# Performance work log

Hardware: AMD Instinct MI355X
Metric: run time of the kernel (lower is better)

## Reference

```python
import math
import jax, jax.numpy as jnp
from jax import lax
import numpy as np

N_LAYERS = 16
MAX_DIL = 128
C_RES = 64
C_DIL = 128
ENC_F = 256
ENC_S = 256
LOOP = int(math.floor(math.log2(MAX_DIL))) + 1  # 8
DILS = [2 ** (i % LOOP) for i in range(N_LAYERS)]  # 1..128 twice


def setup_inputs() -> dict:
    key = jax.random.key(0)
    ks = jax.random.split(key, 9)
    B, T = 8, 131072
    signal = jax.random.normal(ks[0], (B, 1, T), dtype=jnp.float32)
    # params (xavier-ish scales ~ 1/sqrt(fan_in+fan_out))
    W0 = jax.random.normal(ks[1], (C_RES, 1), dtype=jnp.float32) * 0.5          # 1x1 input conv
    b0 = jax.random.normal(ks[2], (C_RES,), dtype=jnp.float32) * 0.02
    Wd = jax.random.normal(ks[3], (N_LAYERS, C_DIL, C_RES, 2), dtype=jnp.float32) * 0.08  # k=2 dilated convs
    bd = jax.random.normal(ks[4], (N_LAYERS, C_DIL), dtype=jnp.float32) * 0.02
    Wr = jax.random.normal(ks[5], (N_LAYERS, C_RES, C_DIL), dtype=jnp.float32) * 0.08     # 1x1 residual convs
    br = jax.random.normal(ks[6], (N_LAYERS, C_RES), dtype=jnp.float32) * 0.02
    Wf = jax.random.normal(ks[7], (1, C_RES), dtype=jnp.float32) * 0.1          # 1x1 final conv
    bf = jax.random.normal(ks[8], (1,), dtype=jnp.float32) * 0.02
    return {"signal": signal, "W0": W0, "b0": b0, "Wd": Wd, "bd": bd,
            "Wr": Wr, "br": br, "Wf": Wf, "bf": bf}


def reference(signal, W0, b0, Wd, bd, Wr, br, Wf, bf):
    # input 1x1 conv: [B,1,T] -> [B,C_RES,T]
    x = jnp.einsum('oi,bit->bot', W0, signal) + b0[None, :, None]
    for i, d in enumerate(DILS):
        skip = x
        h = jax.nn.relu(x)
        # kernel-2 dilated conv, VALID (no causal pad in original): len shrinks by d
        L = h.shape[2]
        h = (jnp.einsum('oc,bct->bot', Wd[i, :, :, 0], h[:, :, :L - d])
             + jnp.einsum('oc,bct->bot', Wd[i, :, :, 1], h[:, :, d:])
             + bd[i][None, :, None])
        h = jax.nn.relu(h)
        # 1x1 residual conv back to C_RES
        h = jnp.einsum('oc,bct->bot', Wr[i], h) + br[i][None, :, None]
        # residual add with right-aligned trim of skip
        x = h + skip[:, :, skip.shape[2] - h.shape[2]:]
    # final 1x1 conv -> [B,1,L']
    x = jnp.einsum('oc,bct->bot', Wf, x) + bf[None, :, None]
    # AvgPool1d(ENC_F, stride=ENC_S), VALID, count_include_pad irrelevant (no pad)
    x = lax.reduce_window(x, 0.0, lax.add, (1, 1, ENC_F), (1, 1, ENC_S), 'VALID') / ENC_F
    return x
```

## Files before the change

### kernel.cpp

```cpp
#include <hip/hip_runtime.h>
#include <hip/hip_bf16.h>
#include <stdint.h>

typedef __attribute__((ext_vector_type(8))) short short8;
typedef __attribute__((ext_vector_type(4))) float f32x4;
typedef unsigned short bfu;

#define T_TILE  128
#define RING    384
#define NTILES  8
#define NLAYERS 16
#define T0LEN   131072
#define BATCH   8
#define RFIELD  510
#define FINLEN  130560
#define CHCAP   65280

#define BARRIER() asm volatile("s_waitcnt lgkmcnt(0)\n\ts_barrier" ::: "memory")

__device__ __forceinline__ bfu f2bf(float f) {
    unsigned u = __float_as_uint(f);
    u += 0x7FFFu + ((u >> 16) & 1u);
    return (bfu)(u >> 16);
}
__device__ __forceinline__ unsigned pk2(float a, float b) {
    __hip_bfloat16 lo = __float2bfloat16(a);
    __hip_bfloat16 hi = __float2bfloat16(b);
    unsigned short ul = __builtin_bit_cast(unsigned short, lo);
    unsigned short uh = __builtin_bit_cast(unsigned short, hi);
    return (unsigned)ul | ((unsigned)uh << 16);
}
__device__ __forceinline__ float bf2f(bfu h) { return __uint_as_float(((unsigned)h) << 16); }
__device__ __forceinline__ unsigned relu2(unsigned w) {
    return w & ~(((w >> 15) & 0x00010001u) * 0xFFFFu);
}

__global__ void prep_weights(const float* __restrict__ Wd, const float* __restrict__ Wr,
                             bfu* __restrict__ wcat, bfu* __restrict__ wrb)
{
    int idx = blockIdx.x * 256 + threadIdx.x;
    const int total1 = NLAYERS * 128 * 128;
    if (idx < total1) {
        int k = idx & 127, o = (idx >> 7) & 127, l = idx >> 14;
        int tap = k >> 6, c = k & 63;
        wcat[idx] = f2bf(Wd[(((l * 128 + o) * 64) + c) * 2 + tap]);
    } else {
        int j = idx - total1;
        if (j < NLAYERS * 64 * 128) wrb[j] = f2bf(Wr[j]);
    }
}

template <int MODE>
__global__ __launch_bounds__(256, 2)
void layer_kernel(const bfu* __restrict__ xin, bfu* __restrict__ xout,
                  const bfu* __restrict__ wcat, const bfu* __restrict__ wrb,
                  const float* __restrict__ bd, const float* __restrict__ br,
                  const float* __restrict__ sig, const float* __restrict__ W0,
                  const float* __restrict__ b0, const float* __restrict__ Wf,
                  float* __restrict__ partial,
                  int s, int d, int Lin, int Lout, int Rrows, int tiles)
{
    __shared__ bfu rx[RING * 64];
    __shared__ bfu hb[128 * 128];

    const int tid  = threadIdx.x;
    const int lane = tid & 63;
    const int wv   = tid >> 6;
    const int l15  = lane & 15;
    const int lg   = lane >> 4;
    const int b    = blockIdx.y;

    const bfu* xb = xin  + (long)b * Rrows * 64;
    bfu*       xo = xout + (long)b * Rrows * 64;
    const float* sgb = sig + (long)b * T0LEN + s;

    short8 a1[2][4];
    #pragma unroll
    for (int m = 0; m < 2; ++m)
        #pragma unroll
        for (int k = 0; k < 4; ++k)
            a1[m][k] = *(const short8*)(wcat + ((wv * 32 + m * 16 + l15) << 7) + (k << 5) + (lg << 3));
    short8 a2[4];
    #pragma unroll
    for (int k = 0; k < 4; ++k)
        a2[k] = *(const short8*)(wrb + ((wv * 16 + l15) << 7) + (k << 5) + (lg << 3));

    const int c0 = wv * 16 + lg * 4;
    const f32x4 brv = *(const f32x4*)(br + c0);
    f32x4 bd4[2];
    #pragma unroll
    for (int m = 0; m < 2; ++m)
        bd4[m] = *(const f32x4*)(bd + wv * 32 + m * 16 + lg * 4);
    f32x4 wfv;
    if constexpr (MODE == 2) wfv = *(const f32x4*)(Wf + c0);

    const int tile0 = blockIdx.x * NTILES;
    const int jmax  = (tiles - tile0 < NTILES) ? (tiles - tile0) : NTILES;
    const int t00   = tile0 * T_TILE;

    if constexpr (MODE == 1) {
        const int nsl = (T_TILE + 1) * 8;
        #pragma unroll
        for (int it = 0; it < 5; ++it) {
            int i = tid + it * 256;
            if (i < nsl) {
                int r = i >> 3, oc = i & 7;
                int t = t00 + r; if (t > Lin - 1) t = Lin - 1;
                float sv = sgb[t];
                unsigned pk[4];
                #pragma unroll
                for (int kk = 0; kk < 4; ++kk) {
                    int c = oc * 8 + kk * 2;
                    pk[kk] = pk2(fmaxf(W0[c] * sv + b0[c], 0.f),
                                 fmaxf(W0[c + 1] * sv + b0[c + 1], 0.f));
                }
                int rs = (t00 + r) % RING;
                uint4 u; u.x = pk[0]; u.y = pk[1]; u.z = pk[2]; u.w = pk[3];
                *(uint4*)&rx[(rs << 6) + ((oc ^ (rs & 7)) << 3)] = u;
            }
        }
    } else {
        const int nsl = (T_TILE + d) * 8;
        uint4 pv[8];
        #pragma unroll
        for (int it = 0; it < 8; ++it) {
            int i = tid + it * 256;
            if (i < nsl) {
                int r = i >> 3, oc = i & 7;
                long t = t00 + r; if (t > Lin - 1) t = Lin - 1;
                pv[it] = *(const uint4*)(xb + t * 64 + oc * 8);
            }
        }
        #pragma unroll
        for (int it = 0; it < 8; ++it) {
            int i = tid + it * 256;
            if (i < nsl) {
                int r = i >> 3, oc = i & 7;
                int rs = (t00 + r) % RING;
                uint4 v = pv[it];
                v.x = relu2(v.x); v.y = relu2(v.y); v.z = relu2(v.z); v.w = relu2(v.w);
                *(uint4*)&rx[(rs << 6) + ((oc ^ (rs & 7)) << 3)] = v;
            }
        }
    }

    for (int j = 0; j < jmax; ++j) {
        const int t0    = t00 + j * T_TILE;
        const int base0 = t0 % RING;
        const int rbase = t0 + T_TILE + d;

        BARRIER();

        uint4 pf[4];
        float pfs[4];
        const bool havePF = (j + 1 < jmax);
        if (havePF) {
            if constexpr (MODE == 1) {
                #pragma unroll
                for (int it = 0; it < 4; ++it) {
                    int i = tid + it * 256;
                    int t = rbase + (i >> 3); if (t > Lin - 1) t = Lin - 1;
                    pfs[it] = sgb[t];
                }
            } else {
                #pragma unroll
                for (int it = 0; it < 4; ++it) {
                    int i = tid + it * 256;
                    int oc = i & 7;
                    long t = rbase + (i >> 3); if (t > Lin - 1) t = Lin - 1;
                    pf[it] = *(const uint4*)(xb + t * 64 + oc * 8);
                }
            }
        }

        uint2 sk[8];
        float skv[8];
        if constexpr (MODE == 1) {
            #pragma unroll
            for (int n = 0; n < 8; ++n) {
                int t = t0 + n * 16 + l15;
                skv[n] = (t < Lout) ? sgb[t + d] : 0.f;
            }
        } else {
            #pragma unroll
            for (int n = 0; n < 8; ++n) {
                int t = t0 + n * 16 + l15;
                uint2 z = {0u, 0u};
                sk[n] = (t < Lout) ? *(const uint2*)(xb + (long)(t + d) * 64 + c0) : z;
            }
        }

        f32x4 acc[2][8] = {};
        #pragma unroll
        for (int k = 0; k < 4; ++k) {
            const int roff = (k >> 1) ? d : 0;
            const int g    = ((k & 1) << 2) + lg;
            #pragma unroll
            for (int n = 0; n < 8; ++n) {
                int rr = base0 + n * 16 + l15 + roff;
                if (rr >= RING) rr -= RING;
                short8 bv = *(const short8*)&rx[(rr << 6) + ((g ^ (rr & 7)) << 3)];
                acc[0][n] = __builtin_amdgcn_mfma_f32_16x16x32_bf16(a1[0][k], bv, acc[0][n], 0, 0, 0);
                acc[1][n] = __builtin_amdgcn_mfma_f32_16x16x32_bf16(a1[1][k], bv, acc[1][n], 0, 0, 0);
            }
        }

        #pragma unroll
        for (int m = 0; m < 2; ++m) {
            const int o0 = wv * 32 + m * 16 + lg * 4;
            const int gg = o0 >> 3;
            #pragma unroll
            for (int n = 0; n < 8; ++n) {
                int t = n * 16 + l15;
                f32x4 h = acc[m][n];
                unsigned q01 = pk2(fmaxf(h.x + bd4[m].x, 0.f), fmaxf(h.y + bd4[m].y, 0.f));
                unsigned q23 = pk2(fmaxf(h.z + bd4[m].z, 0.f), fmaxf(h.w + bd4[m].w, 0.f));
                int idx = (t << 7) + (((gg ^ (t & 15)) << 3) | (o0 & 7));
                uint2 pk; pk.x = q01; pk.y = q23;
                *(uint2*)&hb[idx] = pk;
            }
        }

        if (havePF) {
            if constexpr (MODE == 1) {
                #pragma unroll
                for (int it = 0; it < 4; ++it) {
                    int i = tid + it * 256;
                    int r = i >> 3, oc = i & 7;
                    float sv = pfs[it];
                    unsigned pk[4];
                    #pragma unroll
                    for (int kk = 0; kk < 4; ++kk) {
                        int c = oc * 8 + kk * 2;
                        pk[kk] = pk2(fmaxf(W0[c] * sv + b0[c], 0.f),
                                     fmaxf(W0[c + 1] * sv + b0[c + 1], 0.f));
                    }
                    int rs = (rbase + r) % RING;
                    uint4 u; u.x = pk[0]; u.y = pk[1]; u.z = pk[2]; u.w = pk[3];
                    *(uint4*)&rx[(rs << 6) + ((oc ^ (rs & 7)) << 3)] = u;
                }
            } else {
                #pragma unroll
                for (int it = 0; it < 4; ++it) {
                    int i = tid + it * 256;
                    int r = i >> 3, oc = i & 7;
                    int rs = (rbase + r) % RING;
                    uint4 v = pf[it];
                    v.x = relu2(v.x); v.y = relu2(v.y); v.z = relu2(v.z); v.w = relu2(v.w);
                    *(uint4*)&rx[(rs << 6) + ((oc ^ (rs & 7)) << 3)] = v;
                }
            }
        }

        BARRIER();

        f32x4 acc2[8] = {};
        #pragma unroll
        for (int k = 0; k < 4; ++k) {
            const int g = (k << 2) + lg;
            #pragma unroll
            for (int n = 0; n < 8; ++n) {
                int t = n * 16 + l15;
                short8 bfm = *(const short8*)&hb[(t << 7) + ((g ^ (t & 15)) << 3)];
                acc2[n] = __builtin_amdgcn_mfma_f32_16x16x32_bf16(a2[k], bfm, acc2[n], 0, 0, 0);
            }
        }

        float psum = 0.f;
        #pragma unroll
        for (int n = 0; n < 8; ++n) {
            int t = t0 + n * 16 + l15;
            if (t < Lout) {
                float s0, s1, s2, s3;
                if constexpr (MODE == 1) {
                    float sv = skv[n];
                    s0 = W0[c0] * sv + b0[c0];         s1 = W0[c0 + 1] * sv + b0[c0 + 1];
                    s2 = W0[c0 + 2] * sv + b0[c0 + 2]; s3 = W0[c0 + 3] * sv + b0[c0 + 3];
                } else {
                    s0 = bf2f((bfu)(sk[n].x & 0xFFFF)); s1 = bf2f((bfu)(sk[n].x >> 16));
                    s2 = bf2f((bfu)(sk[n].y & 0xFFFF)); s3 = bf2f((bfu)(sk[n].y >> 16));
                }
                float y0 = acc2[n].x + brv.x + s0;
                float y1 = acc2[n].y + brv.y + s1;
                float y2 = acc2[n].z + brv.z + s2;
                float y3 = acc2[n].w + brv.w + s3;
                if constexpr (MODE == 2) {
                    psum += wfv.x * y0 + wfv.y * y1 + wfv.z * y2 + wfv.w * y3;
                } else {
                    uint2 pk;
                    pk.x = pk2(y0, y1);
                    pk.y = pk2(y2, y3);
                    *(uint2*)(xo + (long)t * 64 + c0) = pk;
                }
            }
        }
        if constexpr (MODE == 2) {
            #pragma unroll
            for (int off = 32; off > 0; off >>= 1) psum += __shfl_down(psum, off, 64);
            if (lane == 0)
                partial[((long)b * 1024 + ((s + t0) >> 7)) * 4 + wv] = psum;
        }
    }
}

__global__ void pool_reduce(const float* __restrict__ part, const float* __restrict__ bfp,
                            float* __restrict__ out)
{
    int i = blockIdx.x * 256 + threadIdx.x;
    if (i >= BATCH * 510) return;
    int b = i / 510, w = i % 510;
    const float* p = part + ((long)b * 1024 + 2 * w) * 4;
    float sum = p[0] + p[1] + p[2] + p[3] + p[4] + p[5] + p[6] + p[7];
    out[i] = sum * (1.0f / 256.0f) + bfp[0];
}

extern "C" void kernel_launch(void* const* d_in, const int* in_sizes, int n_in,
                              void* d_out, int out_size, void* d_ws, size_t ws_size,
                              hipStream_t stream) {
    const float* sig = (const float*)d_in[0];
    const float* W0  = (const float*)d_in[1];
    const float* b0  = (const float*)d_in[2];
    const float* Wd  = (const float*)d_in[3];
    const float* bd  = (const float*)d_in[4];
    const float* Wr  = (const float*)d_in[5];
    const float* br  = (const float*)d_in[6];
    const float* Wf  = (const float*)d_in[7];
    const float* bf  = (const float*)d_in[8];
    float* out = (float*)d_out;

    char* ws = (char*)d_ws;
    const size_t WCAT_E = (size_t)NLAYERS * 128 * 128;
    const size_t WRB_E  = (size_t)NLAYERS * 64 * 128;
    const size_t WBYTES = (WCAT_E + WRB_E) * 2;
    const size_t PARTB  = (size_t)BATCH * 1024 * 4 * 4;
    bfu*   wcat    = (bfu*)ws;
    bfu*   wrb     = (bfu*)(ws + WCAT_E * 2);
    float* partial = (float*)(ws + WBYTES);

    if (ws_size < WBYTES + PARTB + (size_t)2 * BATCH * 766 * 64 * 2) return;

    size_t avail   = ws_size - WBYTES - PARTB;
    long   rowsMax = (long)(avail / ((size_t)2 * BATCH * 64 * 2));
    long   CH      = ((rowsMax - RFIELD) / 256) * 256;
    if (CH > CHCAP) CH = CHCAP;
    if (CH < 256)   CH = 256;
    const long Rrows = CH + RFIELD;

    bfu* xA = (bfu*)(ws + WBYTES + PARTB);
    bfu* xB = xA + (size_t)BATCH * Rrows * 64;

    const int totw = (int)(WCAT_E + WRB_E);
    prep_weights<<<(totw + 255) / 256, 256, 0, stream>>>(Wd, Wr, wcat, wrb);

    bfu* bufs[2] = {xA, xB};
    for (long s = 0; s < FINLEN; s += CH) {
        long CHc  = (FINLEN - s < CH) ? (FINLEN - s) : CH;
        int  len0 = (int)(CHc + RFIELD);

        int cur = 0;
        int L = len0;
        for (int i = 0; i < NLAYERS; ++i) {
            int d = 1 << (i & 7);
            int Lout = L - d;
            int tiles = (Lout + T_TILE - 1) / T_TILE;
            int bx    = (tiles + NTILES - 1) / NTILES;
            dim3 grid(bx, BATCH);
            const bfu* xi = bufs[cur];
            bfu*       xo = bufs[cur ^ 1];
            const bfu* wc  = wcat + (size_t)i * 128 * 128;
            const bfu* wr2 = wrb  + (size_t)i * 64 * 128;
            const float* bdl = bd + i * 128;
            const float* brl = br + i * 64;
            if (i == 0)
                layer_kernel<1><<<grid, 256, 0, stream>>>(xi, xo, wc, wr2, bdl, brl,
                    sig, W0, b0, Wf, partial, (int)s, d, L, Lout, (int)Rrows, tiles);
            else if (i == NLAYERS - 1)
                layer_kernel<2><<<grid, 256, 0, stream>>>(xi, xo, wc, wr2, bdl, brl,
                    sig, W0, b0, Wf, partial, (int)s, d, L, Lout, (int)Rrows, tiles);
            else
                layer_kernel<0><<<grid, 256, 0, stream>>>(xi, xo, wc, wr2, bdl, brl,
                    sig, W0, b0, Wf, partial, (int)s, d, L, Lout, (int)Rrows, tiles);
            cur ^= 1;
            L = Lout;
        }
    }
    pool_reduce<<<(BATCH * 510 + 255) / 256, 256, 0, stream>>>(partial, bf, out);
}
```

Baseline: 1.714 ms.

## Split each time tile across two wave groups with 512-thread blocks

Doubles the block to 512 threads (8 waves). Waves 0-3 cover the same output-channel slices as before, and the wave index's high bit selects which half of the 128-step time tile each wave processes. Per-thread accumulators, skip loads and prefetch registers are halved, which should lower register pressure and raise the waves available to hide LDS and global latency. In exchange the shared-memory footprint per block stays the same. The partial-sum buffer doubles to 8 slots per tile, and pool_reduce sums 16 entries.

```diff
diff --git a/kernel.cpp b/kernel.cpp
--- a/kernel.cpp
+++ b/kernel.cpp
@@ -51,7 +51,7 @@
 }
 
 template <int MODE>
-__global__ __launch_bounds__(256, 2)
+__global__ __launch_bounds__(512, 4)
 void layer_kernel(const bfu* __restrict__ xin, bfu* __restrict__ xout,
                   const bfu* __restrict__ wcat, const bfu* __restrict__ wrb,
                   const float* __restrict__ bd, const float* __restrict__ br,
@@ -66,6 +66,8 @@
     const int tid  = threadIdx.x;
     const int lane = tid & 63;
     const int wv   = tid >> 6;
+    const int m2   = wv & 3;
+    const int th   = wv >> 2;
     const int l15  = lane & 15;
     const int lg   = lane >> 4;
     const int b    = blockIdx.y;
@@ -79,18 +81,18 @@
     for (int m = 0; m < 2; ++m)
         #pragma unroll
         for (int k = 0; k < 4; ++k)
-            a1[m][k] = *(const short8*)(wcat + ((wv * 32 + m * 16 + l15) << 7) + (k << 5) + (lg << 3));
+            a1[m][k] = *(const short8*)(wcat + ((m2 * 32 + m * 16 + l15) << 7) + (k << 5) + (lg << 3));
     short8 a2[4];
     #pragma unroll
     for (int k = 0; k < 4; ++k)
-        a2[k] = *(const short8*)(wrb + ((wv * 16 + l15) << 7) + (k << 5) + (lg << 3));
-
-    const int c0 = wv * 16 + lg * 4;
+        a2[k] = *(const short8*)(wrb + ((m2 * 16 + l15) << 7) + (k << 5) + (lg << 3));
+
+    const int c0 = m2 * 16 + lg * 4;
     const f32x4 brv = *(const f32x4*)(br + c0);
     f32x4 bd4[2];
     #pragma unroll
     for (int m = 0; m < 2; ++m)
-        bd4[m] = *(const f32x4*)(bd + wv * 32 + m * 16 + lg * 4);
+        bd4[m] = *(const f32x4*)(bd + m2 * 32 + m * 16 + lg * 4);
     f32x4 wfv;
     if constexpr (MODE == 2) wfv = *(const f32x4*)(Wf + c0);
 
@@ -101,8 +103,8 @@
     if constexpr (MODE == 1) {
         const int nsl = (T_TILE + 1) * 8;
         #pragma unroll
-        for (int it = 0; it < 5; ++it) {
-            int i = tid + it * 256;
+        for (int it = 0; it < 3; ++it) {
+            int i = tid + it * 512;
             if (i < nsl) {
                 int r = i >> 3, oc = i & 7;
                 int t = t00 + r; if (t > Lin - 1) t = Lin - 1;
@@ -121,10 +123,10 @@
         }
     } else {
         const int nsl = (T_TILE + d) * 8;
-        uint4 pv[8];
-        #pragma unroll
-        for (int it = 0; it < 8; ++it) {
-            int i = tid + it * 256;
+        uint4 pv[4];
+        #pragma unroll
+        for (int it = 0; it < 4; ++it) {
+            int i = tid + it * 512;
             if (i < nsl) {
                 int r = i >> 3, oc = i & 7;
                 long t = t00 + r; if (t > Lin - 1) t = Lin - 1;
@@ -132,8 +134,8 @@
             }
         }
         #pragma unroll
-        for (int it = 0; it < 8; ++it) {
-            int i = tid + it * 256;
+        for (int it = 0; it < 4; ++it) {
+            int i = tid + it * 512;
             if (i < nsl) {
                 int r = i >> 3, oc = i & 7;
                 int rs = (t00 + r) % RING;
@@ -151,21 +153,21 @@
 
         BARRIER();
 
-        uint4 pf[4];
-        float pfs[4];
+        uint4 pf[2];
+        float pfs[2];
         const bool havePF = (j + 1 < jmax);
         if (havePF) {
             if constexpr (MODE == 1) {
                 #pragma unroll
-                for (int it = 0; it < 4; ++it) {
-                    int i = tid + it * 256;
+                for (int it = 0; it < 2; ++it) {
+                    int i = tid + it * 512;
                     int t = rbase + (i >> 3); if (t > Lin - 1) t = Lin - 1;
                     pfs[it] = sgb[t];
                 }
             } else {
                 #pragma unroll
-                for (int it = 0; it < 4; ++it) {
-                    int i = tid + it * 256;
+                for (int it = 0; it < 2; ++it) {
+                    int i = tid + it * 512;
                     int oc = i & 7;
                     long t = rbase + (i >> 3); if (t > Lin - 1) t = Lin - 1;
                     pf[it] = *(const uint4*)(xb + t * 64 + oc * 8);
@@ -173,31 +175,31 @@
             }
         }
 
-        uint2 sk[8];
-        float skv[8];
+        uint2 sk[4];
+        float skv[4];
         if constexpr (MODE == 1) {
             #pragma unroll
-            for (int n = 0; n < 8; ++n) {
-                int t = t0 + n * 16 + l15;
+            for (int n = 0; n < 4; ++n) {
+                int t = t0 + th * 64 + n * 16 + l15;
                 skv[n] = (t < Lout) ? sgb[t + d] : 0.f;
             }
         } else {
             #pragma unroll
-            for (int n = 0; n < 8; ++n) {
-                int t = t0 + n * 16 + l15;
+            for (int n = 0; n < 4; ++n) {
+                int t = t0 + th * 64 + n * 16 + l15;
                 uint2 z = {0u, 0u};
                 sk[n] = (t < Lout) ? *(const uint2*)(xb + (long)(t + d) * 64 + c0) : z;
             }
         }
 
-        f32x4 acc[2][8] = {};
+        f32x4 acc[2][4] = {};
         #pragma unroll
         for (int k = 0; k < 4; ++k) {
             const int roff = (k >> 1) ? d : 0;
             const int g    = ((k & 1) << 2) + lg;
             #pragma unroll
-            for (int n = 0; n < 8; ++n) {
-                int rr = base0 + n * 16 + l15 + roff;
+            for (int n = 0; n < 4; ++n) {
+                int rr = base0 + th * 64 + n * 16 + l15 + roff;
                 if (rr >= RING) rr -= RING;
                 short8 bv = *(const short8*)&rx[(rr << 6) + ((g ^ (rr & 7)) << 3)];
                 acc[0][n] = __builtin_amdgcn_mfma_f32_16x16x32_bf16(a1[0][k], bv, acc[0][n], 0, 0, 0);
@@ -207,15 +209,15 @@
 
         #pragma unroll
         for (int m = 0; m < 2; ++m) {
-            const int o0 = wv * 32 + m * 16 + lg * 4;
+            const int o0 = m2 * 32 + m * 16 + lg * 4;
             const int gg = o0 >> 3;
             #pragma unroll
-            for (int n = 0; n < 8; ++n) {
-                int t = n * 16 + l15;
+            for (int n = 0; n < 4; ++n) {
+                int tl = th * 64 + n * 16 + l15;
                 f32x4 h = acc[m][n];
                 unsigned q01 = pk2(fmaxf(h.x + bd4[m].x, 0.f), fmaxf(h.y + bd4[m].y, 0.f));
                 unsigned q23 = pk2(fmaxf(h.z + bd4[m].z, 0.f), fmaxf(h.w + bd4[m].w, 0.f));
-                int idx = (t << 7) + (((gg ^ (t & 15)) << 3) | (o0 & 7));
+                int idx = (tl << 7) + (((gg ^ (tl & 15)) << 3) | (o0 & 7));
                 uint2 pk; pk.x = q01; pk.y = q23;
                 *(uint2*)&hb[idx] = pk;
             }
@@ -224,8 +226,8 @@
         if (havePF) {
             if constexpr (MODE == 1) {
                 #pragma unroll
-                for (int it = 0; it < 4; ++it) {
-                    int i = tid + it * 256;
+                for (int it = 0; it < 2; ++it) {
+                    int i = tid + it * 512;
                     int r = i >> 3, oc = i & 7;
                     float sv = pfs[it];
                     unsigned pk[4];
@@ -241,8 +243,8 @@
                 }
             } else {
                 #pragma unroll
-                for (int it = 0; it < 4; ++it) {
-                    int i = tid + it * 256;
+                for (int it = 0; it < 2; ++it) {
+                    int i = tid + it * 512;
                     int r = i >> 3, oc = i & 7;
                     int rs = (rbase + r) % RING;
                     uint4 v = pf[it];
@@ -254,22 +256,22 @@
 
         BARRIER();
 
-        f32x4 acc2[8] = {};
+        f32x4 acc2[4] = {};
         #pragma unroll
         for (int k = 0; k < 4; ++k) {
             const int g = (k << 2) + lg;
             #pragma unroll
-            for (int n = 0; n < 8; ++n) {
-                int t = n * 16 + l15;
-                short8 bfm = *(const short8*)&hb[(t << 7) + ((g ^ (t & 15)) << 3)];
+            for (int n = 0; n < 4; ++n) {
+                int tl = th * 64 + n * 16 + l15;
+                short8 bfm = *(const short8*)&hb[(tl << 7) + ((g ^ (tl & 15)) << 3)];
                 acc2[n] = __builtin_amdgcn_mfma_f32_16x16x32_bf16(a2[k], bfm, acc2[n], 0, 0, 0);
             }
         }
 
         float psum = 0.f;
         #pragma unroll
-        for (int n = 0; n < 8; ++n) {
-            int t = t0 + n * 16 + l15;
+        for (int n = 0; n < 4; ++n) {
+            int t = t0 + th * 64 + n * 16 + l15;
             if (t < Lout) {
                 float s0, s1, s2, s3;
                 if constexpr (MODE == 1) {
@@ -298,7 +300,7 @@
             #pragma unroll
             for (int off = 32; off > 0; off >>= 1) psum += __shfl_down(psum, off, 64);
             if (lane == 0)
-                partial[((long)b * 1024 + ((s + t0) >> 7)) * 4 + wv] = psum;
+                partial[((long)b * 1024 + ((s + t0) >> 7)) * 8 + wv] = psum;
         }
     }
 }
@@ -309,8 +311,10 @@
     int i = blockIdx.x * 256 + threadIdx.x;
     if (i >= BATCH * 510) return;
     int b = i / 510, w = i % 510;
-    const float* p = part + ((long)b * 1024 + 2 * w) * 4;
-    float sum = p[0] + p[1] + p[2] + p[3] + p[4] + p[5] + p[6] + p[7];
+    const float* p = part + ((long)b * 1024 + 2 * w) * 8;
+    float sum = 0.f;
+    #pragma unroll
+    for (int q = 0; q < 16; ++q) sum += p[q];
     out[i] = sum * (1.0f / 256.0f) + bfp[0];
 }
 
@@ -332,7 +336,7 @@
     const size_t WCAT_E = (size_t)NLAYERS * 128 * 128;
     const size_t WRB_E  = (size_t)NLAYERS * 64 * 128;
     const size_t WBYTES = (WCAT_E + WRB_E) * 2;
-    const size_t PARTB  = (size_t)BATCH * 1024 * 4 * 4;
+    const size_t PARTB  = (size_t)BATCH * 1024 * 8 * 4;
     bfu*   wcat    = (bfu*)ws;
     bfu*   wrb     = (bfu*)(ws + WCAT_E * 2);
     float* partial = (float*)(ws + WBYTES);
@@ -372,13 +376,13 @@
             const float* bdl = bd + i * 128;
             const float* brl = br + i * 64;
             if (i == 0)
-                layer_kernel<1><<<grid, 256, 0, stream>>>(xi, xo, wc, wr2, bdl, brl,
+                layer_kernel<1><<<grid, 512, 0, stream>>>(xi, xo, wc, wr2, bdl, brl,
                     sig, W0, b0, Wf, partial, (int)s, d, L, Lout, (int)Rrows, tiles);
             else if (i == NLAYERS - 1)
-                layer_kernel<2><<<grid, 256, 0, stream>>>(xi, xo, wc, wr2, bdl, brl,
+                layer_kernel<2><<<grid, 512, 0, stream>>>(xi, xo, wc, wr2, bdl, brl,
                     sig, W0, b0, Wf, partial, (int)s, d, L, Lout, (int)Rrows, tiles);
             else
-                layer_kernel<0><<<grid, 256, 0, stream>>>(xi, xo, wc, wr2, bdl, brl,
+                layer_kernel<0><<<grid, 512, 0, stream>>>(xi, xo, wc, wr2, bdl, brl,
                     sig, W0, b0, Wf, partial, (int)s, d, L, Lout, (int)Rrows, tiles);
             cur ^= 1;
             L = Lout;
```

Result: slower. 2.617 ms (+52.7%).
